# Kernel optimization log

Hardware: AMD Instinct MI355X
Metric: run time of the kernel (lower is better)

Reference implementation:

```python
import jax, jax.numpy as jnp
import numpy as np
from functools import partial

EPS = 1e-5
CFGS = [(128, 0.02, 32), (64, 0.04, 32), (32, 0.08, 16)]  # (npoint, radius, nsample)
DIMS = [(9, 32), (32, 64), (67, 128), (128, 128), (131, 256), (256, 256)]  # per-layer (Cin, Cout)


def _fps(xyz, npoint):
    # xyz: (N,3). Farthest point sampling, deterministic start at index 0 (pointnet2 convention).
    N = xyz.shape[0]
    def body(carry, _):
        dist, last = carry
        d = jnp.sum((xyz - xyz[last]) ** 2, axis=-1)
        dist = jnp.minimum(dist, d)
        nxt = jnp.argmax(dist).astype(jnp.int32)
        return (dist, nxt), nxt
    init = (jnp.full((N,), 1e10, xyz.dtype), jnp.int32(0))
    _, rest = jax.lax.scan(body, init, None, length=npoint - 1)
    return jnp.concatenate([jnp.zeros((1,), jnp.int32), rest])


def _ball_query(new_xyz, xyz, radius, nsample):
    # new_xyz: (S,3), xyz: (N,3) -> (S, nsample) int32 indices.
    # pointnet2 semantics: first `nsample` in-order points within radius; pad with first hit.
    N = xyz.shape[0]
    d2 = jnp.sum((new_xyz[:, None, :] - xyz[None, :, :]) ** 2, axis=-1)  # (S,N)
    cand = jnp.where(d2 < radius * radius, jnp.arange(N, dtype=jnp.int32)[None, :], N)
    srt = jnp.sort(cand, axis=-1)[:, :nsample]
    first = srt[:, :1]
    first = jnp.where(first == N, 0, first)
    return jnp.where(srt == N, first, srt)


def _sa(xyz, feats, npoint, radius, nsample, layers):
    # xyz: (B,N,3), feats: (B,C,N)
    fps_idx = jax.vmap(partial(_fps, npoint=npoint))(xyz)                       # (B,S)
    new_xyz = jnp.take_along_axis(xyz, fps_idx[..., None].astype(jnp.int32), axis=1)  # (B,S,3)
    idx = jax.vmap(partial(_ball_query, radius=radius, nsample=nsample))(new_xyz, xyz)  # (B,S,ns)
    g_xyz = jax.vmap(lambda x, i: x[i])(xyz, idx) - new_xyz[:, :, None, :]      # (B,S,ns,3) relative
    g_feat = jax.vmap(lambda f, i: f[:, i])(feats, idx)                         # (B,C,S,ns)
    x = jnp.concatenate([g_xyz.transpose(0, 3, 1, 2), g_feat], axis=1)          # (B,3+C,S,ns)
    for (w, g, b, m, v) in layers:  # 1x1 conv + eval-mode BN + ReLU
        x = jnp.einsum('oc,bcsn->bosn', w, x)
        x = g[:, None, None] * (x - m[:, None, None]) * jax.lax.rsqrt(v + EPS)[:, None, None] + b[:, None, None]
        x = jax.nn.relu(x)
    return new_xyz, jnp.max(x, axis=-1)  # (B,S,3), (B,Cout,S)


def _forward(pc, flat):
    layers = [tuple(flat[i * 5:(i + 1) * 5]) for i in range(6)]
    xyz = pc
    feats = jnp.concatenate([pc, pc], axis=-1).transpose(0, 2, 1)  # (B,6,N)
    for k, (npoint, radius, nsample) in enumerate(CFGS):
        xyz, feats = _sa(xyz, feats, npoint, radius, nsample, layers[2 * k:2 * k + 2])
    return feats  # (B,256,32)


def setup_inputs() -> dict:
    key = jax.random.key(0)
    ks = jax.random.split(key, 64)
    d = {"pc": jax.random.uniform(ks[0], (64, 4096, 3), dtype=jnp.float32) * 0.1}
    ki = 1
    for li, (cin, cout) in enumerate(DIMS):
        d[f"w{li}"] = jax.random.normal(ks[ki], (cout, cin), jnp.float32) / np.sqrt(cin).astype(np.float32); ki += 1
        d[f"g{li}"] = jax.random.uniform(ks[ki], (cout,), jnp.float32, 0.5, 1.5); ki += 1
        d[f"be{li}"] = jax.random.normal(ks[ki], (cout,), jnp.float32) * 0.05; ki += 1
        d[f"rm{li}"] = jax.random.normal(ks[ki], (cout,), jnp.float32) * 0.05; ki += 1
        d[f"rv{li}"] = jax.random.uniform(ks[ki], (cout,), jnp.float32, 0.5, 1.5); ki += 1
    return d


def reference(pc, w0, g0, be0, rm0, rv0, w1, g1, be1, rm1, rv1,
              w2, g2, be2, rm2, rv2, w3, g3, be3, rm3, rv3,
              w4, g4, be4, rm4, rv4, w5, g5, be5, rm5, rv5):
    flat = (w0, g0, be0, rm0, rv0, w1, g1, be1, rm1, rv1,
            w2, g2, be2, rm2, rv2, w3, g3, be3, rm3, rv3,
            w4, g4, be4, rm4, rv4, w5, g5, be5, rm5, rv5)
    return _forward(pc, flat)
```

## Files before the change

### kernel.cpp

```cpp
#include <hip/hip_runtime.h>
#include <math.h>


struct PrepArgs {
  const float* w[6]; const float* g[6]; const float* be[6];
  const float* rm[6]; const float* rv[6];
};

__device__ __forceinline__ void prep_body(const PrepArgs& a, float* __restrict__ wT,
                                          float* __restrict__ bias, int i) {
  const int woff[7] = {0, 384, 2432, 11136, 27520, 61312, 126848};
  const int cin[6]  = {9, 32, 67, 128, 131, 256};
  const int osh[6]  = {5, 6, 7, 7, 8, 8};
  const int boff[7] = {0, 32, 96, 224, 352, 608, 864};
  if (i < 126848) {
    int l = 0;
    while (i >= woff[l + 1]) ++l;
    int local = i - woff[l];
    int c = local >> osh[l];
    int o = local & ((1 << osh[l]) - 1);
    float sc = a.g[l][o] / sqrtf(a.rv[l][o] + 1e-5f);
    wT[i] = (c < cin[l]) ? a.w[l][o * cin[l] + c] * sc : 0.f;
  } else if (i < 127712) {
    int j = i - 126848;
    int l = 0;
    while (j >= boff[l + 1]) ++l;
    int o = j - boff[l];
    float sc = a.g[l][o] / sqrtf(a.rv[l][o] + 1e-5f);
    bias[j] = a.be[l][o] - a.rm[l][o] * sc;
  }
}

__device__ __forceinline__ float dist2_exact(float px, float py, float pz,
                                             float cx, float cy, float cz) {
  float dx = px - cx, dy = py - cy, dz = pz - cz;
  return __fadd_rn(__fadd_rn(__fmul_rn(dx, dx), __fmul_rn(dy, dy)), __fmul_rn(dz, dz));
}

__device__ __forceinline__ float wave_max64(float v) {
  #pragma unroll
  for (int off = 32; off >= 1; off >>= 1)
    v = fmaxf(v, __shfl_xor(v, (unsigned)off, 64));
  return v;
}

__global__ __launch_bounds__(256) void fps1_prep_kernel(const float* __restrict__ pc,
    float* __restrict__ newxyz, PrepArgs pa, float* __restrict__ wT,
    float* __restrict__ bias) {
  int t = threadIdx.x;
  if (blockIdx.x >= 64) {
    prep_body(pa, wT, bias, (int)(blockIdx.x - 64) * 256 + t);
    return;
  }
  int b = blockIdx.x;
  const float* xb = pc + (size_t)b * 4096 * 3;
  float* out = newxyz + (size_t)b * 128 * 3;
  __shared__ float s_pts[4096 * 3];
  __shared__ float s_v[2][4];
  __shared__ int s_i[2][4];
  for (int e = t; e < 4096 * 3; e += 256) s_pts[e] = xb[e];
  __syncthreads();
  float px[16], py[16], pz[16], dist[16];
  #pragma unroll
  for (int k = 0; k < 16; ++k) {
    int i = t * 16 + k;
    px[k] = s_pts[i * 3]; py[k] = s_pts[i * 3 + 1]; pz[k] = s_pts[i * 3 + 2];
    dist[k] = 1e10f;
  }
  float cx = s_pts[0], cy = s_pts[1], cz = s_pts[2];
  if (t == 0) { out[0] = cx; out[1] = cy; out[2] = cz; }
  int lane = t & 63, wv = t >> 6, base = t * 16;
  for (int it = 1; it < 128; ++it) {
    float bv = -1.f; int lidx = base;
    #pragma unroll
    for (int k = 0; k < 16; ++k) {
      float d = dist2_exact(px[k], py[k], pz[k], cx, cy, cz);
      float nd = fminf(dist[k], d);
      dist[k] = nd;
      if (nd > bv) { bv = nd; lidx = base + k; }
    }
    float wm = wave_max64(bv);
    unsigned long long m = __ballot(bv == wm);
    int src = __ffsll(m) - 1;
    int widx = __shfl(lidx, src, 64);
    int pb = it & 1;
    if (lane == 0) { s_v[pb][wv] = wm; s_i[pb][wv] = widx; }
    __syncthreads();
    float v0 = s_v[pb][0]; int i0 = s_i[pb][0];
    #pragma unroll
    for (int w = 1; w < 4; ++w) {
      float v = s_v[pb][w]; int ii = s_i[pb][w];
      if (v > v0 || (v == v0 && ii < i0)) { v0 = v; i0 = ii; }
    }
    cx = s_pts[i0 * 3]; cy = s_pts[i0 * 3 + 1]; cz = s_pts[i0 * 3 + 2];
    if (t == 0) { out[it * 3] = cx; out[it * 3 + 1] = cy; out[it * 3 + 2] = cz; }
  }
}

__device__ __forceinline__ void fps2_body(const float* __restrict__ xyz1,
                                          float* __restrict__ out_xyz, int b, int t) {
  const float* xb = xyz1 + (size_t)b * 128 * 3;
  float* out = out_xyz + (size_t)b * 64 * 3;
  float px[2], py[2], pz[2], dist[2];
  #pragma unroll
  for (int k = 0; k < 2; ++k) {
    int i = t * 2 + k;
    px[k] = xb[i * 3]; py[k] = xb[i * 3 + 1]; pz[k] = xb[i * 3 + 2];
    dist[k] = 1e10f;
  }
  float cx = __shfl(px[0], 0, 64), cy = __shfl(py[0], 0, 64), cz = __shfl(pz[0], 0, 64);
  if (t == 0) { out[0] = cx; out[1] = cy; out[2] = cz; }
  for (int it = 1; it < 64; ++it) {
    float bv = -1.f; int lidx = t * 2;
    #pragma unroll
    for (int k = 0; k < 2; ++k) {
      float d = dist2_exact(px[k], py[k], pz[k], cx, cy, cz);
      float nd = fminf(dist[k], d);
      dist[k] = nd;
      if (nd > bv) { bv = nd; lidx = t * 2 + k; }
    }
    float wm = wave_max64(bv);
    unsigned long long m = __ballot(bv == wm);
    int src = __ffsll(m) - 1;
    int widx = __shfl(lidx, src, 64);
    int sl = widx >> 1, sk = widx & 1;
    float qx = sk ? px[1] : px[0], qy = sk ? py[1] : py[0], qz = sk ? pz[1] : pz[0];
    cx = __shfl(qx, sl, 64); cy = __shfl(qy, sl, 64); cz = __shfl(qz, sl, 64);
    if (t == 0) { out[it * 3] = cx; out[it * 3 + 1] = cy; out[it * 3 + 2] = cz; }
  }
}

__device__ __forceinline__ void fps3_body(const float* __restrict__ xyz2,
                                          float* __restrict__ out_xyz, int b, int t) {
  const float* xb = xyz2 + (size_t)b * 64 * 3;
  float* out = out_xyz + (size_t)b * 32 * 3;
  float px = xb[t * 3], py = xb[t * 3 + 1], pz = xb[t * 3 + 2];
  float dist = 1e10f;
  float cx = __shfl(px, 0, 64), cy = __shfl(py, 0, 64), cz = __shfl(pz, 0, 64);
  if (t == 0) { out[0] = cx; out[1] = cy; out[2] = cz; }
  for (int it = 1; it < 32; ++it) {
    float d = dist2_exact(px, py, pz, cx, cy, cz);
    dist = fminf(dist, d);
    float wm = wave_max64(dist);
    unsigned long long m = __ballot(dist == wm);
    int widx = __ffsll(m) - 1;
    cx = __shfl(px, widx, 64); cy = __shfl(py, widx, 64); cz = __shfl(pz, widx, 64);
    if (t == 0) { out[it * 3] = cx; out[it * 3 + 1] = cy; out[it * 3 + 2] = cz; }
  }
}

__device__ __forceinline__ int ball_query_wave(const float* __restrict__ xb, int N,
                                               float cx, float cy, float cz, float r2,
                                               int nsample, int* list, int lane) {
  int cnt = 0;
  for (int base = 0; base < N && cnt < nsample; base += 64) {
    int i = base + lane;
    float d2 = dist2_exact(xb[i * 3], xb[i * 3 + 1], xb[i * 3 + 2], cx, cy, cz);
    bool in = d2 < r2;
    unsigned long long m = __ballot(in);
    if (in) {
      int pos = cnt + __popcll(m & ((1ull << lane) - 1ull));
      if (pos < nsample) list[pos] = i;
    }
    cnt += __popcll(m);
  }
  return cnt;
}

#define FMA4(aq, w0, w1, w2, w3, xv, comp)                                   \
  aq = fmaf(w0.comp, xv.x, fmaf(w1.comp, xv.y, fmaf(w2.comp, xv.z,           \
       fmaf(w3.comp, xv.w, aq))))

__global__ __launch_bounds__(256) void group1_fps2_kernel(const float* __restrict__ pc,
    const float* __restrict__ newxyz1, const float* __restrict__ wbuf,
    const float* __restrict__ bbuf, float* __restrict__ U1,
    float* __restrict__ xyz2) {
  int t = threadIdx.x;
  int b = blockIdx.y;
  if (blockIdx.x == 16) {
    if (t < 64) fps2_body(newxyz1, xyz2, b, t);
    return;
  }
  __shared__ float W0s[384];
  __shared__ float W1s[2048];
  __shared__ float X[128 * 12];
  __shared__ float h1[128 * 36];
  __shared__ float pm1[16 * 64];
  __shared__ float F1[4 * 64];
  __shared__ float ctr[24];
  __shared__ int lst[256];
  __shared__ int cnts[8];
  int s0 = blockIdx.x * 8;
  const float* xb = pc + (size_t)b * 4096 * 3;
  const float* W2g = wbuf + 2432;
  for (int e = t; e < 384; e += 256) W0s[e] = wbuf[e];
  for (int e = t; e < 2048; e += 256) W1s[e] = wbuf[384 + e];
  int lane = t & 63, wv = t >> 6;
  for (int k = 0; k < 2; ++k) {
    int g = wv * 2 + k;
    const float* c3 = newxyz1 + ((size_t)b * 128 + s0 + g) * 3;
    float cx = c3[0], cy = c3[1], cz = c3[2];
    if (lane == 0) { ctr[g * 3] = cx; ctr[g * 3 + 1] = cy; ctr[g * 3 + 2] = cz; }
    int cnt = ball_query_wave(xb, 4096, cx, cy, cz, 4.0e-4f, 32, lst + g * 32, lane);
    if (lane == 0) cnts[g] = cnt;
  }
  __syncthreads();
  { int g = t >> 5, q = t & 31; if (q >= cnts[g]) lst[t] = (cnts[g] > 0) ? lst[g * 32] : 0; }
  __syncthreads();
  int o_l0 = t & 31, jb0 = (t >> 5) * 16;
  float w0v[12];
  #pragma unroll
  for (int c = 0; c < 12; ++c) w0v[c] = W0s[c * 32 + o_l0];
  float b0 = bbuf[o_l0];
  int ot1 = t & 15, jt1 = t >> 4;
  int o0 = ot1 * 4, j0 = jt1 * 8;
  float bias1[4];
  #pragma unroll
  for (int r = 0; r < 4; ++r) bias1[r] = bbuf[32 + o0 + r];
  for (int chunk = 0; chunk < 2; ++chunk) {
    if (t < 128) {
      int j = t;
      int g = chunk * 4 + (j >> 5);
      int i = lst[g * 32 + (j & 31)];
      float px = xb[i * 3], py = xb[i * 3 + 1], pz = xb[i * 3 + 2];
      float4 v0, v1, v2;
      v0.x = px - ctr[g * 3]; v0.y = py - ctr[g * 3 + 1]; v0.z = pz - ctr[g * 3 + 2];
      v0.w = px; v1.x = py; v1.y = pz; v1.z = px; v1.w = py;
      v2.x = pz; v2.y = 0.f; v2.z = 0.f; v2.w = 0.f;
      *reinterpret_cast<float4*>(&X[j * 12 + 0]) = v0;
      *reinterpret_cast<float4*>(&X[j * 12 + 4]) = v1;
      *reinterpret_cast<float4*>(&X[j * 12 + 8]) = v2;
    }
    __syncthreads();
    for (int jj = 0; jj < 16; ++jj) {
      int j = jb0 + jj;
      float4 x0 = *reinterpret_cast<const float4*>(&X[j * 12 + 0]);
      float4 x1 = *reinterpret_cast<const float4*>(&X[j * 12 + 4]);
      float4 x2 = *reinterpret_cast<const float4*>(&X[j * 12 + 8]);
      float a = b0;
      a = fmaf(w0v[0], x0.x, a); a = fmaf(w0v[1], x0.y, a);
      a = fmaf(w0v[2], x0.z, a); a = fmaf(w0v[3], x0.w, a);
      a = fmaf(w0v[4], x1.x, a); a = fmaf(w0v[5], x1.y, a);
      a = fmaf(w0v[6], x1.z, a); a = fmaf(w0v[7], x1.w, a);
      a = fmaf(w0v[8], x2.x, a); a = fmaf(w0v[9], x2.y, a);
      a = fmaf(w0v[10], x2.z, a); a = fmaf(w0v[11], x2.w, a);
      h1[j * 36 + o_l0] = fmaxf(a, 0.f);
    }
    __syncthreads();
    float acc[8][4];
    #pragma unroll
    for (int q = 0; q < 8; ++q)
      #pragma unroll
      for (int r = 0; r < 4; ++r) acc[q][r] = bias1[r];
    for (int c4 = 0; c4 < 8; ++c4) {
      int c = c4 * 4;
      float4 w0 = *reinterpret_cast<const float4*>(&W1s[(c + 0) * 64 + o0]);
      float4 w1 = *reinterpret_cast<const float4*>(&W1s[(c + 1) * 64 + o0]);
      float4 w2 = *reinterpret_cast<const float4*>(&W1s[(c + 2) * 64 + o0]);
      float4 w3 = *reinterpret_cast<const float4*>(&W1s[(c + 3) * 64 + o0]);
      #pragma unroll
      for (int q = 0; q < 8; ++q) {
        float4 xv = *reinterpret_cast<const float4*>(&h1[(j0 + q) * 36 + c]);
        FMA4(acc[q][0], w0, w1, w2, w3, xv, x);
        FMA4(acc[q][1], w0, w1, w2, w3, xv, y);
        FMA4(acc[q][2], w0, w1, w2, w3, xv, z);
        FMA4(acc[q][3], w0, w1, w2, w3, xv, w);
      }
    }
    {
      float m[4] = {-1e30f, -1e30f, -1e30f, -1e30f};
      #pragma unroll
      for (int q = 0; q < 8; ++q)
        #pragma unroll
        for (int r = 0; r < 4; ++r) m[r] = fmaxf(m[r], acc[q][r]);
      float4 mv; mv.x = m[0]; mv.y = m[1]; mv.z = m[2]; mv.w = m[3];
      *reinterpret_cast<float4*>(&pm1[jt1 * 64 + o0]) = mv;
    }
    __syncthreads();
    {
      int o = t & 63, g = t >> 6;
      float v = pm1[(4 * g + 0) * 64 + o];
      v = fmaxf(v, pm1[(4 * g + 1) * 64 + o]);
      v = fmaxf(v, pm1[(4 * g + 2) * 64 + o]);
      v = fmaxf(v, pm1[(4 * g + 3) * 64 + o]);
      F1[g * 64 + o] = fmaxf(v, 0.f);
    }
    __syncthreads();
    {
      int o = t & 127, ph = t >> 7;
      float a0 = bbuf[96 + o], a1 = a0;
      #pragma unroll 8
      for (int c = 0; c < 64; ++c) {
        float w = W2g[(3 + c) * 128 + o];
        a0 = fmaf(w, F1[ph * 64 + c], a0);
        a1 = fmaf(w, F1[(ph + 2) * 64 + c], a1);
      }
      int sA = s0 + chunk * 4;
      U1[((size_t)b * 128 + sA + ph) * 128 + o] = a0;
      U1[((size_t)b * 128 + sA + ph + 2) * 128 + o] = a1;
    }
    __syncthreads();
  }
}

__global__ __launch_bounds__(256) void group2_fps3_kernel(const float* __restrict__ xyz1,
    const float* __restrict__ newxyz2, const float* __restrict__ U1,
    const float* __restrict__ wbuf, const float* __restrict__ bbuf,
    float* __restrict__ U2, float* __restrict__ xyz3) {
  int t = threadIdx.x;
  int b = blockIdx.y;
  if (blockIdx.x == 16) {
    if (t < 64) fps3_body(newxyz2, xyz3, b, t);
    return;
  }
  __shared__ float Hs[64 * 132];
  __shared__ float D[64 * 4];
  __shared__ float W2x[384];
  __shared__ float pm[8 * 128];
  __shared__ float F2[2 * 128];
  __shared__ float ctr[12];
  __shared__ int lst[128];
  __shared__ int cnts[4];
  int s0 = blockIdx.x * 4;
  const float* xb = xyz1 + (size_t)b * 128 * 3;
  const float* W2g = wbuf + 2432;
  const float* W3g = wbuf + 11136;
  const float* W4g = wbuf + 27520;
  int lane = t & 63, wv = t >> 6;
  for (int e = t; e < 384; e += 256) W2x[e] = W2g[e];
  {
    int g = wv;
    const float* c3 = newxyz2 + ((size_t)b * 64 + s0 + g) * 3;
    float cx = c3[0], cy = c3[1], cz = c3[2];
    if (lane == 0) { ctr[g * 3] = cx; ctr[g * 3 + 1] = cy; ctr[g * 3 + 2] = cz; }
    int cnt = ball_query_wave(xb, 128, cx, cy, cz, 1.6e-3f, 32, lst + g * 32, lane);
    if (lane == 0) cnts[g] = cnt;
  }
  __syncthreads();
  if (t < 128) { int g = t >> 5, q = t & 31; if (q >= cnts[g]) lst[t] = (cnts[g] > 0) ? lst[g * 32] : 0; }
  __syncthreads();
  int ot = t & 31, jt = t >> 5;
  int o0 = ot * 4, j0 = jt * 8;
  float4 wx0 = *reinterpret_cast<const float4*>(&W2x[0 * 128 + o0]);
  float4 wx1 = *reinterpret_cast<const float4*>(&W2x[1 * 128 + o0]);
  float4 wx2 = *reinterpret_cast<const float4*>(&W2x[2 * 128 + o0]);
  float bias3[4];
  #pragma unroll
  for (int r = 0; r < 4; ++r) bias3[r] = bbuf[224 + o0 + r];
  for (int chunk = 0; chunk < 2; ++chunk) {
    if (t < 64) {
      int j = t;
      int g = chunk * 2 + (j >> 5);
      int i = lst[g * 32 + (j & 31)];
      D[j * 4 + 0] = xb[i * 3 + 0] - ctr[g * 3 + 0];
      D[j * 4 + 1] = xb[i * 3 + 1] - ctr[g * 3 + 1];
      D[j * 4 + 2] = xb[i * 3 + 2] - ctr[g * 3 + 2];
      D[j * 4 + 3] = 0.f;
    }
    __syncthreads();
    #pragma unroll
    for (int q = 0; q < 8; ++q) {
      int j = j0 + q;
      int g = chunk * 2 + (j >> 5);
      int i = lst[g * 32 + (j & 31)];
      float4 u = *reinterpret_cast<const float4*>(&U1[((size_t)b * 128 + i) * 128 + o0]);
      float dx = D[j * 4], dy = D[j * 4 + 1], dz = D[j * 4 + 2];
      float4 h;
      h.x = fmaf(wx0.x, dx, fmaf(wx1.x, dy, fmaf(wx2.x, dz, u.x)));
      h.y = fmaf(wx0.y, dx, fmaf(wx1.y, dy, fmaf(wx2.y, dz, u.y)));
      h.z = fmaf(wx0.z, dx, fmaf(wx1.z, dy, fmaf(wx2.z, dz, u.z)));
      h.w = fmaf(wx0.w, dx, fmaf(wx1.w, dy, fmaf(wx2.w, dz, u.w)));
      h.x = fmaxf(h.x, 0.f); h.y = fmaxf(h.y, 0.f);
      h.z = fmaxf(h.z, 0.f); h.w = fmaxf(h.w, 0.f);
      *reinterpret_cast<float4*>(&Hs[j * 132 + o0]) = h;
    }
    __syncthreads();
    float acc[8][4];
    #pragma unroll
    for (int q = 0; q < 8; ++q)
      #pragma unroll
      for (int r = 0; r < 4; ++r) acc[q][r] = bias3[r];
    for (int c4 = 0; c4 < 32; ++c4) {
      int c = c4 * 4;
      float4 w0 = *reinterpret_cast<const float4*>(&W3g[(c + 0) * 128 + o0]);
      float4 w1 = *reinterpret_cast<const float4*>(&W3g[(c + 1) * 128 + o0]);
      float4 w2 = *reinterpret_cast<const float4*>(&W3g[(c + 2) * 128 + o0]);
      float4 w3 = *reinterpret_cast<const float4*>(&W3g[(c + 3) * 128 + o0]);
      #pragma unroll
      for (int q = 0; q < 8; ++q) {
        float4 xv = *reinterpret_cast<const float4*>(&Hs[(j0 + q) * 132 + c]);
        FMA4(acc[q][0], w0, w1, w2, w3, xv, x);
        FMA4(acc[q][1], w0, w1, w2, w3, xv, y);
        FMA4(acc[q][2], w0, w1, w2, w3, xv, z);
        FMA4(acc[q][3], w0, w1, w2, w3, xv, w);
      }
    }
    {
      float m[4] = {-1e30f, -1e30f, -1e30f, -1e30f};
      #pragma unroll
      for (int q = 0; q < 8; ++q)
        #pragma unroll
        for (int r = 0; r < 4; ++r) m[r] = fmaxf(m[r], acc[q][r]);
      float4 mv; mv.x = m[0]; mv.y = m[1]; mv.z = m[2]; mv.w = m[3];
      *reinterpret_cast<float4*>(&pm[jt * 128 + o0]) = mv;
    }
    __syncthreads();
    {
      int o = t & 127, g = t >> 7;
      float v = pm[(g * 4 + 0) * 128 + o];
      v = fmaxf(v, pm[(g * 4 + 1) * 128 + o]);
      v = fmaxf(v, pm[(g * 4 + 2) * 128 + o]);
      v = fmaxf(v, pm[(g * 4 + 3) * 128 + o]);
      F2[g * 128 + o] = fmaxf(v, 0.f);
    }
    __syncthreads();
    {
      int o = t;
      float a0 = bbuf[352 + o], a1 = a0;
      #pragma unroll 4
      for (int c = 0; c < 128; ++c) {
        float w = W4g[(3 + c) * 256 + o];
        a0 = fmaf(w, F2[c], a0);
        a1 = fmaf(w, F2[128 + c], a1);
      }
      int sA = s0 + chunk * 2;
      U2[((size_t)b * 64 + sA) * 256 + o] = a0;
      U2[((size_t)b * 64 + sA + 1) * 256 + o] = a1;
    }
    __syncthreads();
  }
}

__global__ __launch_bounds__(256) void group3_kernel(const float* __restrict__ xyz2,
    const float* __restrict__ newxyz3, const float* __restrict__ U2,
    const float* __restrict__ wbuf, const float* __restrict__ bbuf,
    float* __restrict__ out) {
  __shared__ float Hs3[32 * 260];
  __shared__ float D[32 * 4];
  __shared__ float W4x[768];
  __shared__ float pm3[4 * 256];
  __shared__ float ctr[6];
  __shared__ int lst[32];
  __shared__ int cnts[2];
  int t = threadIdx.x;
  int b = blockIdx.y, s0 = blockIdx.x * 2;
  const float* xb = xyz2 + (size_t)b * 64 * 3;
  const float* W4g = wbuf + 27520;
  const float* W5g = wbuf + 61312;
  int lane = t & 63, wv = t >> 6;
  for (int e = t; e < 768; e += 256) W4x[e] = W4g[e];
  if (wv < 2) {
    int g = wv;
    const float* c3 = newxyz3 + ((size_t)b * 32 + s0 + g) * 3;
    float cx = c3[0], cy = c3[1], cz = c3[2];
    if (lane == 0) { ctr[g * 3] = cx; ctr[g * 3 + 1] = cy; ctr[g * 3 + 2] = cz; }
    int cnt = ball_query_wave(xb, 64, cx, cy, cz, 6.4e-3f, 16, lst + g * 16, lane);
    if (lane == 0) cnts[g] = cnt;
  }
  __syncthreads();
  if (t < 32) { int g = t >> 4, q = t & 15; if (q >= cnts[g]) lst[t] = (cnts[g] > 0) ? lst[g * 16] : 0; }
  __syncthreads();
  int ot = t & 63, jt = t >> 6;
  int o0 = ot * 4, j0 = jt * 8;
  float4 wx0 = *reinterpret_cast<const float4*>(&W4x[0 * 256 + o0]);
  float4 wx1 = *reinterpret_cast<const float4*>(&W4x[1 * 256 + o0]);
  float4 wx2 = *reinterpret_cast<const float4*>(&W4x[2 * 256 + o0]);
  float bias5[4];
  #pragma unroll
  for (int r = 0; r < 4; ++r) bias5[r] = bbuf[608 + o0 + r];
  if (t < 32) {
    int j = t;
    int g = j >> 4;
    int i = lst[g * 16 + (j & 15)];
    D[j * 4 + 0] = xb[i * 3 + 0] - ctr[g * 3 + 0];
    D[j * 4 + 1] = xb[i * 3 + 1] - ctr[g * 3 + 1];
    D[j * 4 + 2] = xb[i * 3 + 2] - ctr[g * 3 + 2];
    D[j * 4 + 3] = 0.f;
  }
  __syncthreads();
  #pragma unroll
  for (int q = 0; q < 8; ++q) {
    int j = j0 + q;
    int g = j >> 4;
    int i = lst[g * 16 + (j & 15)];
    float4 u = *reinterpret_cast<const float4*>(&U2[((size_t)b * 64 + i) * 256 + o0]);
    float dx = D[j * 4], dy = D[j * 4 + 1], dz = D[j * 4 + 2];
    float4 h;
    h.x = fmaf(wx0.x, dx, fmaf(wx1.x, dy, fmaf(wx2.x, dz, u.x)));
    h.y = fmaf(wx0.y, dx, fmaf(wx1.y, dy, fmaf(wx2.y, dz, u.y)));
    h.z = fmaf(wx0.z, dx, fmaf(wx1.z, dy, fmaf(wx2.z, dz, u.z)));
    h.w = fmaf(wx0.w, dx, fmaf(wx1.w, dy, fmaf(wx2.w, dz, u.w)));
    h.x = fmaxf(h.x, 0.f); h.y = fmaxf(h.y, 0.f);
    h.z = fmaxf(h.z, 0.f); h.w = fmaxf(h.w, 0.f);
    *reinterpret_cast<float4*>(&Hs3[j * 260 + o0]) = h;
  }
  __syncthreads();
  float acc[8][4];
  #pragma unroll
  for (int q = 0; q < 8; ++q)
    #pragma unroll
    for (int r = 0; r < 4; ++r) acc[q][r] = bias5[r];
  for (int c4 = 0; c4 < 64; ++c4) {
    int c = c4 * 4;
    float4 w0 = *reinterpret_cast<const float4*>(&W5g[(c + 0) * 256 + o0]);
    float4 w1 = *reinterpret_cast<const float4*>(&W5g[(c + 1) * 256 + o0]);
    float4 w2 = *reinterpret_cast<const float4*>(&W5g[(c + 2) * 256 + o0]);
    float4 w3 = *reinterpret_cast<const float4*>(&W5g[(c + 3) * 256 + o0]);
    #pragma unroll
    for (int q = 0; q < 8; ++q) {
      float4 xv = *reinterpret_cast<const float4*>(&Hs3[(j0 + q) * 260 + c]);
      FMA4(acc[q][0], w0, w1, w2, w3, xv, x);
      FMA4(acc[q][1], w0, w1, w2, w3, xv, y);
      FMA4(acc[q][2], w0, w1, w2, w3, xv, z);
      FMA4(acc[q][3], w0, w1, w2, w3, xv, w);
    }
  }
  {
    float m[4] = {-1e30f, -1e30f, -1e30f, -1e30f};
    #pragma unroll
    for (int q = 0; q < 8; ++q)
      #pragma unroll
      for (int r = 0; r < 4; ++r) m[r] = fmaxf(m[r], acc[q][r]);
    float4 mv; mv.x = m[0]; mv.y = m[1]; mv.z = m[2]; mv.w = m[3];
    *reinterpret_cast<float4*>(&pm3[jt * 256 + o0]) = mv;
  }
  __syncthreads();
  {
    int o = t;
    #pragma unroll
    for (int g = 0; g < 2; ++g) {
      float v = fmaxf(pm3[(g * 2 + 0) * 256 + o], pm3[(g * 2 + 1) * 256 + o]);
      out[((size_t)b * 256 + o) * 32 + s0 + g] = fmaxf(v, 0.f);
    }
  }
}

extern "C" void kernel_launch(void* const* d_in, const int* in_sizes, int n_in,
                              void* d_out, int out_size, void* d_ws, size_t ws_size,
                              hipStream_t stream) {
  (void)in_sizes; (void)n_in; (void)out_size; (void)ws_size;
  const float* pc = (const float*)d_in[0];
  PrepArgs pa;
  for (int l = 0; l < 6; ++l) {
    pa.w[l]  = (const float*)d_in[1 + 5 * l + 0];
    pa.g[l]  = (const float*)d_in[1 + 5 * l + 1];
    pa.be[l] = (const float*)d_in[1 + 5 * l + 2];
    pa.rm[l] = (const float*)d_in[1 + 5 * l + 3];
    pa.rv[l] = (const float*)d_in[1 + 5 * l + 4];
  }
  float* ws = (float*)d_ws;
  float* wbuf = ws + 0;
  float* bbuf = ws + 126848;
  float* xyz1 = ws + 131072;
  float* xyz2 = ws + 155648;
  float* xyz3 = ws + 167936;
  float* U1   = ws + 174080;
  float* U2   = ws + 1222656;
  float* out  = (float*)d_out;

  fps1_prep_kernel<<<563, 256, 0, stream>>>(pc, xyz1, pa, wbuf, bbuf);
  group1_fps2_kernel<<<dim3(17, 64), 256, 0, stream>>>(pc, xyz1, wbuf, bbuf, U1, xyz2);
  group2_fps3_kernel<<<dim3(17, 64), 256, 0, stream>>>(xyz1, xyz2, U1, wbuf, bbuf, U2, xyz3);
  group3_kernel<<<dim3(16, 64), 256, 0, stream>>>(xyz2, xyz3, U2, wbuf, bbuf, out);
}
```

Before: 443.8 us.

## Speed up FPS reductions with DPP wave max, readlane, and 512-thread blocks

The first FPS kernel now uses 512 threads with 8 points per thread, loads points straight from global memory as float4 instead of staging them in shared memory, and carries the winning coordinates through the reduction so no index lookup is needed. Wave max reductions use DPP row operations plus readlane instead of shuffle-xor chains, and broadcasts use readlane. The goal is a shorter serial critical path per FPS iteration, which is latency-bound with only 64 blocks. The cross-wave tie-break now keeps the first wave on equal maxima instead of comparing indices, which still matches lowest-index semantics because waves are in index order. The DPP reduction depends on specific row and bank masks being correct.

```diff
diff --git a/kernel.cpp b/kernel.cpp
--- a/kernel.cpp
+++ b/kernel.cpp
@@ -37,64 +37,90 @@
   return __fadd_rn(__fadd_rn(__fmul_rn(dx, dx), __fmul_rn(dy, dy)), __fmul_rn(dz, dz));
 }
 
-__device__ __forceinline__ float wave_max64(float v) {
-  #pragma unroll
-  for (int off = 32; off >= 1; off >>= 1)
-    v = fmaxf(v, __shfl_xor(v, (unsigned)off, 64));
+__device__ __forceinline__ float wave_max64_dpp(float v) {
+  int x;
+  x = __builtin_amdgcn_update_dpp(0, __float_as_int(v), 0x111, 0xf, 0xf, true);
+  v = fmaxf(v, __int_as_float(x));
+  x = __builtin_amdgcn_update_dpp(0, __float_as_int(v), 0x112, 0xf, 0xf, true);
+  v = fmaxf(v, __int_as_float(x));
+  x = __builtin_amdgcn_update_dpp(0, __float_as_int(v), 0x114, 0xf, 0xf, true);
+  v = fmaxf(v, __int_as_float(x));
+  x = __builtin_amdgcn_update_dpp(0, __float_as_int(v), 0x118, 0xf, 0xf, true);
+  v = fmaxf(v, __int_as_float(x));
+  x = __builtin_amdgcn_update_dpp(0, __float_as_int(v), 0x142, 0xa, 0xf, true);
+  v = fmaxf(v, __int_as_float(x));
+  x = __builtin_amdgcn_update_dpp(0, __float_as_int(v), 0x143, 0xc, 0xf, true);
+  v = fmaxf(v, __int_as_float(x));
   return v;
 }
-
-__global__ __launch_bounds__(256) void fps1_prep_kernel(const float* __restrict__ pc,
+__device__ __forceinline__ float rl_f(float v, int lane) {
+  return __int_as_float(__builtin_amdgcn_readlane(__float_as_int(v), lane));
+}
+
+__global__ __launch_bounds__(512) void fps1_prep_kernel(const float* __restrict__ pc,
     float* __restrict__ newxyz, PrepArgs pa, float* __restrict__ wT,
     float* __restrict__ bias) {
   int t = threadIdx.x;
   if (blockIdx.x >= 64) {
-    prep_body(pa, wT, bias, (int)(blockIdx.x - 64) * 256 + t);
+    prep_body(pa, wT, bias, (int)(blockIdx.x - 64) * 512 + t);
     return;
   }
   int b = blockIdx.x;
   const float* xb = pc + (size_t)b * 4096 * 3;
   float* out = newxyz + (size_t)b * 128 * 3;
-  __shared__ float s_pts[4096 * 3];
-  __shared__ float s_v[2][4];
-  __shared__ int s_i[2][4];
-  for (int e = t; e < 4096 * 3; e += 256) s_pts[e] = xb[e];
-  __syncthreads();
-  float px[16], py[16], pz[16], dist[16];
-  #pragma unroll
-  for (int k = 0; k < 16; ++k) {
-    int i = t * 16 + k;
-    px[k] = s_pts[i * 3]; py[k] = s_pts[i * 3 + 1]; pz[k] = s_pts[i * 3 + 2];
-    dist[k] = 1e10f;
-  }
-  float cx = s_pts[0], cy = s_pts[1], cz = s_pts[2];
-  if (t == 0) { out[0] = cx; out[1] = cy; out[2] = cz; }
-  int lane = t & 63, wv = t >> 6, base = t * 16;
+  __shared__ float candf[2][8][4];
+  __shared__ float out_lds[128 * 3];
+  float px[8], py[8], pz[8], dist[8];
+  {
+    float fl[24];
+    const float4* xb4 = reinterpret_cast<const float4*>(xb + t * 24);
+    #pragma unroll
+    for (int u = 0; u < 6; ++u) {
+      float4 L = xb4[u];
+      fl[4 * u] = L.x; fl[4 * u + 1] = L.y; fl[4 * u + 2] = L.z; fl[4 * u + 3] = L.w;
+    }
+    #pragma unroll
+    for (int k = 0; k < 8; ++k) {
+      px[k] = fl[3 * k]; py[k] = fl[3 * k + 1]; pz[k] = fl[3 * k + 2];
+      dist[k] = 1e10f;
+    }
+  }
+  float cx = xb[0], cy = xb[1], cz = xb[2];
+  if (t == 0) { out_lds[0] = cx; out_lds[1] = cy; out_lds[2] = cz; }
+  int lane = t & 63, wv = t >> 6, base = t * 8;
   for (int it = 1; it < 128; ++it) {
-    float bv = -1.f; int lidx = base;
-    #pragma unroll
-    for (int k = 0; k < 16; ++k) {
+    float bv = -1.f, bx = px[0], by = py[0], bz = pz[0];
+    #pragma unroll
+    for (int k = 0; k < 8; ++k) {
       float d = dist2_exact(px[k], py[k], pz[k], cx, cy, cz);
       float nd = fminf(dist[k], d);
       dist[k] = nd;
-      if (nd > bv) { bv = nd; lidx = base + k; }
-    }
-    float wm = wave_max64(bv);
+      bool up = nd > bv;
+      bv = up ? nd : bv;
+      bx = up ? px[k] : bx; by = up ? py[k] : by; bz = up ? pz[k] : bz;
+    }
+    float wm = rl_f(wave_max64_dpp(bv), 63);
     unsigned long long m = __ballot(bv == wm);
     int src = __ffsll(m) - 1;
-    int widx = __shfl(lidx, src, 64);
     int pb = it & 1;
-    if (lane == 0) { s_v[pb][wv] = wm; s_i[pb][wv] = widx; }
-    __syncthreads();
-    float v0 = s_v[pb][0]; int i0 = s_i[pb][0];
-    #pragma unroll
-    for (int w = 1; w < 4; ++w) {
-      float v = s_v[pb][w]; int ii = s_i[pb][w];
-      if (v > v0 || (v == v0 && ii < i0)) { v0 = v; i0 = ii; }
-    }
-    cx = s_pts[i0 * 3]; cy = s_pts[i0 * 3 + 1]; cz = s_pts[i0 * 3 + 2];
-    if (t == 0) { out[it * 3] = cx; out[it * 3 + 1] = cy; out[it * 3 + 2] = cz; }
-  }
+    if (lane == src) {
+      candf[pb][wv][0] = bv; candf[pb][wv][1] = bx;
+      candf[pb][wv][2] = by; candf[pb][wv][3] = bz;
+    }
+    __syncthreads();
+    float4 bc = *reinterpret_cast<const float4*>(&candf[pb][0][0]);
+    #pragma unroll
+    for (int w = 1; w < 8; ++w) {
+      float4 cw = *reinterpret_cast<const float4*>(&candf[pb][w][0]);
+      bool up = cw.x > bc.x;
+      bc.x = up ? cw.x : bc.x; bc.y = up ? cw.y : bc.y;
+      bc.z = up ? cw.z : bc.z; bc.w = up ? cw.w : bc.w;
+    }
+    cx = bc.y; cy = bc.z; cz = bc.w;
+    if (t == 0) { out_lds[it * 3] = cx; out_lds[it * 3 + 1] = cy; out_lds[it * 3 + 2] = cz; }
+  }
+  __syncthreads();
+  for (int e = t; e < 384; e += 512) out[e] = out_lds[e];
 }
 
 __device__ __forceinline__ void fps2_body(const float* __restrict__ xyz1,
@@ -108,7 +134,7 @@
     px[k] = xb[i * 3]; py[k] = xb[i * 3 + 1]; pz[k] = xb[i * 3 + 2];
     dist[k] = 1e10f;
   }
-  float cx = __shfl(px[0], 0, 64), cy = __shfl(py[0], 0, 64), cz = __shfl(pz[0], 0, 64);
+  float cx = rl_f(px[0], 0), cy = rl_f(py[0], 0), cz = rl_f(pz[0], 0);
   if (t == 0) { out[0] = cx; out[1] = cy; out[2] = cz; }
   for (int it = 1; it < 64; ++it) {
     float bv = -1.f; int lidx = t * 2;
@@ -119,13 +145,13 @@
       dist[k] = nd;
       if (nd > bv) { bv = nd; lidx = t * 2 + k; }
     }
-    float wm = wave_max64(bv);
+    float wm = rl_f(wave_max64_dpp(bv), 63);
     unsigned long long m = __ballot(bv == wm);
     int src = __ffsll(m) - 1;
-    int widx = __shfl(lidx, src, 64);
+    int widx = __builtin_amdgcn_readlane(lidx, src);
     int sl = widx >> 1, sk = widx & 1;
     float qx = sk ? px[1] : px[0], qy = sk ? py[1] : py[0], qz = sk ? pz[1] : pz[0];
-    cx = __shfl(qx, sl, 64); cy = __shfl(qy, sl, 64); cz = __shfl(qz, sl, 64);
+    cx = rl_f(qx, sl); cy = rl_f(qy, sl); cz = rl_f(qz, sl);
     if (t == 0) { out[it * 3] = cx; out[it * 3 + 1] = cy; out[it * 3 + 2] = cz; }
   }
 }
@@ -136,15 +162,15 @@
   float* out = out_xyz + (size_t)b * 32 * 3;
   float px = xb[t * 3], py = xb[t * 3 + 1], pz = xb[t * 3 + 2];
   float dist = 1e10f;
-  float cx = __shfl(px, 0, 64), cy = __shfl(py, 0, 64), cz = __shfl(pz, 0, 64);
+  float cx = rl_f(px, 0), cy = rl_f(py, 0), cz = rl_f(pz, 0);
   if (t == 0) { out[0] = cx; out[1] = cy; out[2] = cz; }
   for (int it = 1; it < 32; ++it) {
     float d = dist2_exact(px, py, pz, cx, cy, cz);
     dist = fminf(dist, d);
-    float wm = wave_max64(dist);
+    float wm = rl_f(wave_max64_dpp(dist), 63);
     unsigned long long m = __ballot(dist == wm);
     int widx = __ffsll(m) - 1;
-    cx = __shfl(px, widx, 64); cy = __shfl(py, widx, 64); cz = __shfl(pz, widx, 64);
+    cx = rl_f(px, widx); cy = rl_f(py, widx); cz = rl_f(pz, widx);
     if (t == 0) { out[it * 3] = cx; out[it * 3 + 1] = cy; out[it * 3 + 2] = cz; }
   }
 }
@@ -558,7 +584,7 @@
   float* U2   = ws + 1222656;
   float* out  = (float*)d_out;
 
-  fps1_prep_kernel<<<563, 256, 0, stream>>>(pc, xyz1, pa, wbuf, bbuf);
+  fps1_prep_kernel<<<314, 512, 0, stream>>>(pc, xyz1, pa, wbuf, bbuf);
   group1_fps2_kernel<<<dim3(17, 64), 256, 0, stream>>>(pc, xyz1, wbuf, bbuf, U1, xyz2);
   group2_fps3_kernel<<<dim3(17, 64), 256, 0, stream>>>(xyz1, xyz2, U1, wbuf, bbuf, U2, xyz3);
   group3_kernel<<<dim3(16, 64), 256, 0, stream>>>(xyz2, xyz3, U2, wbuf, bbuf, out);
```

New measurement: 426.2 us. -4.0%, faster.
